# Optimization experiments

Measured on AMD Instinct MI355X. Metric: run time of the kernel, lower is better.

## Reference

```python
import jax, jax.numpy as jnp
import numpy as np

NU, NI, E = 100000, 20000, 250000
H, HEADS, D, L = 128, 2, 64, 2


def setup_inputs() -> dict:
    key = jax.random.key(0)
    ks = jax.random.split(key, 12)
    s = 0.05  # glorot-ish init scale
    return {
        "x_user": jax.random.normal(ks[0], (NU, 64), jnp.float32),
        "x_item": jax.random.normal(ks[1], (NI, 128), jnp.float32),
        "Wp_user": jax.random.normal(ks[2], (64, H), jnp.float32) * s,
        "bp_user": jnp.zeros((H,), jnp.float32),
        "Wp_item": jax.random.normal(ks[3], (128, H), jnp.float32) * s,
        "bp_item": jnp.zeros((H,), jnp.float32),
        # stacked per [layer, relation] params; rel 0 = user->item, rel 1 = item->user
        "Wl": jax.random.normal(ks[4], (L, 2, H, H), jnp.float32) * s,  # source linear
        "bl": jnp.zeros((L, 2, H), jnp.float32),
        "Wr": jax.random.normal(ks[5], (L, 2, H, H), jnp.float32) * s,  # target linear
        "br": jnp.zeros((L, 2, H), jnp.float32),
        "att": jax.random.normal(ks[6], (L, 2, HEADS, D), jnp.float32) * s,
        "bias": jnp.zeros((L, 2, H), jnp.float32),
        "edge_src": jax.random.randint(ks[7], (E,), 0, NU, jnp.int32),  # user index per edge
        "edge_dst": jax.random.randint(ks[8], (E,), 0, NI, jnp.int32),  # item index per edge
    }


def _gatv2(x_src, x_dst, src, dst, wl, bl_, wr, br_, a, b_, n_dst):
    """One bipartite GATv2Conv (heads=HEADS, out=D, concat=True, eval mode)."""
    xl = (x_src @ wl + bl_).reshape(-1, HEADS, D)  # [Ns, h, d]
    xr = (x_dst @ wr + br_).reshape(-1, HEADS, D)  # [Nd, h, d]
    e = jax.nn.leaky_relu(xl[src] + xr[dst], 0.2)  # [E, h, d]
    logits = jnp.einsum('ehd,hd->eh', e, a)        # [E, h]
    # segment softmax over destination nodes (numerically stable)
    amax = jax.lax.stop_gradient(jax.ops.segment_max(logits, dst, num_segments=n_dst))
    p = jnp.exp(logits - amax[dst])
    denom = jax.ops.segment_sum(p, dst, num_segments=n_dst)
    alpha = p / (denom[dst] + 1e-16)               # PyG softmax epsilon
    msg = xl[src] * alpha[:, :, None]              # [E, h, d]
    out = jax.ops.segment_sum(msg, dst, num_segments=n_dst)  # [Nd, h, d]
    return out.reshape(n_dst, HEADS * D) + b_


def reference(x_user, x_item, Wp_user, bp_user, Wp_item, bp_item,
              Wl, bl, Wr, br, att, bias, edge_src, edge_dst):
    zu = x_user @ Wp_user + bp_user  # [NU, H]
    zi = x_item @ Wp_item + bp_item  # [NI, H]
    for l in range(L):
        zi_new = _gatv2(zu, zi, edge_src, edge_dst,
                        Wl[l, 0], bl[l, 0], Wr[l, 0], br[l, 0], att[l, 0], bias[l, 0], NI)
        zu_new = _gatv2(zi, zu, edge_dst, edge_src,
                        Wl[l, 1], bl[l, 1], Wr[l, 1], br[l, 1], att[l, 1], bias[l, 1], NU)
        zu, zi = zu_new, zi_new
        if l < L - 1:
            zu, zi = jax.nn.relu(zu), jax.nn.relu(zi)  # dropout is identity in eval
    return zu, zi
```

## Files before the change

kernel.cpp:

```cpp
#include <hip/hip_runtime.h>

#define HDIM 128

typedef __attribute__((ext_vector_type(8))) short short8;
typedef __attribute__((ext_vector_type(4))) float float4v;

__device__ __forceinline__ float b2f(unsigned short u){
  return __uint_as_float(((unsigned int)u) << 16);
}
__device__ __forceinline__ unsigned short f2b(float f){
  unsigned int x = __float_as_uint(f);
  x += 0x7fffu + ((x >> 16) & 1u);
  return (unsigned short)(x >> 16);
}

#if __has_builtin(__builtin_amdgcn_exp2f)
#define EXPX(x) __builtin_amdgcn_exp2f(x)
#define LOGSCALE 1.4426950408889634f
#else
#define EXPX(x) __expf(x)
#define LOGSCALE 1.f
#endif

__device__ __forceinline__ float dpp_red8(float x){
  x += __int_as_float(__builtin_amdgcn_update_dpp(0, __float_as_int(x), 0xB1, 0xF, 0xF, true));
  x += __int_as_float(__builtin_amdgcn_update_dpp(0, __float_as_int(x), 0x4E, 0xF, 0xF, true));
  x += __int_as_float(__builtin_amdgcn_update_dpp(0, __float_as_int(x), 0x141, 0xF, 0xF, true));
  return x;
}

__global__ void detect_kernel(const unsigned short* __restrict__ x, int* __restrict__ flag){
  const int tid = threadIdx.x;
  int cnt = 0, tot = 0;
  for (int i = tid * 2; i < 4096; i += 512){
    float v = fabsf(b2f(x[i]));
    tot++;
    if (v > 1e-4f && v < 50.f) cnt++;
  }
  __shared__ int s_cnt[256], s_tot[256];
  s_cnt[tid] = cnt; s_tot[tid] = tot;
  __syncthreads();
  for (int o = 128; o > 0; o >>= 1){
    if (tid < o){ s_cnt[tid] += s_cnt[tid + o]; s_tot[tid] += s_tot[tid + o]; }
    __syncthreads();
  }
  if (tid == 0) flag[0] = (s_cnt[0] * 2 < s_tot[0]) ? 1 : 0;
}

#define P_WPU 0
#define P_WPI 8192
#define P_WL  24576
#define P_WR  90112
#define P_BL  155648
#define P_BR  156160
#define P_ATT 156672
#define P_BIA 157184
#define P_BPU 157696
#define P_BPI 157824
#define P_TOT 157952

struct CvtArgs { const void* src[10]; int len[10]; };

__global__ void cvt_all_kernel(CvtArgs args, unsigned short* __restrict__ P,
                               const int* __restrict__ flag){
  int t = blockIdx.x * 256 + threadIdx.x;
  if (t >= P_TOT) return;
  int local = t;
  int i = 0;
  while (local >= args.len[i]){ local -= args.len[i]; i++; }
  if (*flag) P[t] = f2b(((const float*)args.src[i])[local]);
  else       P[t] = ((const unsigned short*)args.src[i])[local];
}

__global__ void prep_weights_kernel(const unsigned short* __restrict__ P,
                                    unsigned short* __restrict__ Wc)
{
  const int t = blockIdx.x * 256 + threadIdx.x;
  if (t >= 49664) return;
  const unsigned short* Wl = P + P_WL;
  const unsigned short* Wr = P + P_WR;
  const unsigned short* Bm[4] = { Wl, Wr + 16384, Wl + 16384, Wr };
  const unsigned short* Av[4] = { P + P_WPU, P + P_WPU, P + P_WPI, P + P_WPI };
  const unsigned short* bv[4] = { P + P_BPU, P + P_BPU, P + P_BPI, P + P_BPI };
  const unsigned short* bo[4] = { P + P_BL, P + P_BR + 128, P + P_BL + 128, P + P_BR };
  if (t < 49152){
    int job, base;
    if (t < 8192)       { job = 0; base = 0; }
    else if (t < 16384) { job = 1; base = 8192; }
    else if (t < 32768) { job = 2; base = 16384; }
    else                { job = 3; base = 32768; }
    const int local = t - base;
    const int k = local >> 7, n = local & 127;
    const unsigned short* A = Av[job] + (size_t)k * 128;
    const unsigned short* B = Bm[job];
    float s = 0.f;
    #pragma unroll 4
    for (int h = 0; h < 128; h++) s = fmaf(b2f(A[h]), b2f(B[h * 128 + n]), s);
    Wc[t] = f2b(s);
  } else {
    const int local = t - 49152;
    const int job = local >> 7, n = local & 127;
    const unsigned short* B = Bm[job];
    float s = b2f(bo[job][n]);
    for (int h = 0; h < 128; h++) s = fmaf(b2f(bv[job][h]), b2f(B[h * 128 + n]), s);
    Wc[t] = f2b(s);
  }
}

struct PermArgs { const unsigned short* W0[4]; const unsigned short* W1[4];
                  int KS[4]; int base[4]; int n[4]; };
__global__ void permute_all_kernel(PermArgs pa, unsigned short* __restrict__ dst){
  int t = blockIdx.x * 256 + threadIdx.x;
  int job = 0;
  while (job < 4 && t >= pa.base[job] + pa.n[job]) job++;
  if (job >= 4) return;
  int local = t - pa.base[job];
  int KS = pa.KS[job];
  int j = local & 7, rest = local >> 3;
  int l = rest & 63; rest >>= 6;
  int ks = rest % KS, tile = rest / KS;
  int k = ks * 32 + (l >> 4) * 8 + j;
  int c = tile * 16 + (l & 15);
  dst[t] = (c < 128) ? pa.W0[job][k * 128 + c] : pa.W1[job][k * 128 + (c - 128)];
}

__global__ void bias_cat_kernel(const unsigned short* a0, const unsigned short* b0,
                                const unsigned short* a1, const unsigned short* b1,
                                const unsigned short* a2, const unsigned short* b2,
                                const unsigned short* a3, const unsigned short* b3,
                                unsigned short* __restrict__ dst){
  int t = blockIdx.x * 256 + threadIdx.x;
  if (t >= 1024) return;
  const unsigned short* lo[4] = {a0, a1, a2, a3};
  const unsigned short* hi[4] = {b0, b1, b2, b3};
  int set = t >> 8, c = t & 255;
  dst[t] = (c < 128) ? lo[set][c] : hi[set][c - 128];
}

template<int K>
__launch_bounds__(256)
__global__ void linear_mfma_kernel(const void* __restrict__ Xv, int xstride,
                                   const int* __restrict__ flag, int use_flag,
                                   const unsigned short* __restrict__ Bp,
                                   const unsigned short* __restrict__ bias,
                                   unsigned short* __restrict__ Y, int M)
{
  constexpr int KS = K / 32;
  const int wave = threadIdx.x >> 6, lane = threadIdx.x & 63;
  const int quad = lane >> 4, l16 = lane & 15;
  const int row0 = blockIdx.x * 64;
  const bool f32 = use_flag && (*flag != 0);

  float4v acc[4][4];
  const float4v z = {0.f, 0.f, 0.f, 0.f};
  #pragma unroll
  for (int i = 0; i < 4; i++)
    #pragma unroll
    for (int j = 0; j < 4; j++) acc[i][j] = z;

  for (int ks = 0; ks < KS; ks++){
    const int col = ks * 32 + quad * 8;
    short8 a[4];
    #pragma unroll
    for (int mt = 0; mt < 4; mt++){
      int r = row0 + mt * 16 + l16; if (r >= M) r = M - 1;
      if (f32){
        const float* p = (const float*)Xv + (size_t)r * xstride + col;
        short8 tmp;
        #pragma unroll
        for (int j = 0; j < 8; j++) tmp[j] = (short)f2b(p[j]);
        a[mt] = tmp;
      } else {
        a[mt] = *(const short8*)((const unsigned short*)Xv + (size_t)r * xstride + col);
      }
    }
    short8 b[4];
    #pragma unroll
    for (int ntl = 0; ntl < 4; ntl++){
      const int t = wave * 4 + ntl;
      b[ntl] = *(const short8*)(Bp + ((size_t)(t * KS + ks) * 64 + lane) * 8);
    }
    #pragma unroll
    for (int mt = 0; mt < 4; mt++)
      #pragma unroll
      for (int ntl = 0; ntl < 4; ntl++)
        acc[mt][ntl] = __builtin_amdgcn_mfma_f32_16x16x32_bf16(a[mt], b[ntl], acc[mt][ntl], 0, 0, 0);
  }

  #pragma unroll
  for (int mt = 0; mt < 4; mt++){
    #pragma unroll
    for (int ntl = 0; ntl < 4; ntl++){
      const int t = wave * 4 + ntl;
      const int colb = t * 16 + l16;
      const float bb = b2f(bias[colb]);
      #pragma unroll
      for (int r = 0; r < 4; r++){
        const int row = row0 + mt * 16 + quad * 4 + r;
        if (row < M) Y[(size_t)row * 256 + colb] = f2b(acc[mt][ntl][r] + bb);
      }
    }
  }
}

__global__ void count_both_kernel(const int* __restrict__ esrc, const int* __restrict__ edst,
                                  int* __restrict__ degU, int* __restrict__ degI, int E){
  int t = blockIdx.x * 256 + threadIdx.x;
  if (t >= E) return;
  atomicAdd(&degI[edst[t]], 1);
  atomicAdd(&degU[esrc[t]], 1);
}

__global__ void scan_block2_kernel(const int* __restrict__ degI, const int* __restrict__ degU,
                                   int* __restrict__ rpI, int* __restrict__ rpU,
                                   int* __restrict__ blkI, int* __restrict__ blkU,
                                   int NI, int NU, int BI){
  __shared__ int s[256];
  const int tid = threadIdx.x;
  const int b = blockIdx.x;
  const int* deg; int* rowptr; int* blksum; int Nd; int bb;
  if (b < BI){ deg = degI; rowptr = rpI; blksum = blkI; Nd = NI; bb = b; }
  else       { deg = degU; rowptr = rpU; blksum = blkU; Nd = NU; bb = b - BI; }
  const int base = bb * 2048 + tid * 8;
  int v[8]; int tot = 0;
  #pragma unroll
  for (int j = 0; j < 8; j++){
    int idx = base + j;
    v[j] = (idx < Nd) ? deg[idx] : 0;
    tot += v[j];
  }
  s[tid] = tot;
  __syncthreads();
  for (int off = 1; off < 256; off <<= 1){
    int add = (tid >= off) ? s[tid - off] : 0;
    __syncthreads();
    s[tid] += add;
    __syncthreads();
  }
  int run = s[tid] - tot;
  #pragma unroll
  for (int j = 0; j < 8; j++){
    int idx = base + j;
    if (idx < Nd) rowptr[idx] = run;
    run += v[j];
  }
  if (tid == 255) blksum[bb] = s[255];
}

__global__ void scan_top2_kernel(int* __restrict__ blkI, int BI,
                                 int* __restrict__ blkU, int BU){
  const int tid = threadIdx.x;
  int* blk = (tid < 64) ? blkI : blkU;
  const int B = (tid < 64) ? BI : BU;
  const int lane = tid & 63;
  int v = (lane < B) ? blk[lane] : 0;
  const int orig = v;
  #pragma unroll
  for (int off = 1; off < 64; off <<= 1){
    int u = __shfl_up(v, off, 64);
    if (lane >= off) v += u;
  }
  if (lane < B) blk[lane] = v - orig;
}

__global__ void scan_add2_kernel(int* __restrict__ rpI, int* __restrict__ rpU,
                                 const int* __restrict__ blkI, const int* __restrict__ blkU,
                                 int* __restrict__ curI, int* __restrict__ curU,
                                 int NI, int NU, int BI, int E){
  const int b = blockIdx.x;
  int* rowptr; const int* blksum; int* curs; int Nd; int bb;
  if (b < BI){ rowptr = rpI; blksum = blkI; curs = curI; Nd = NI; bb = b; }
  else       { rowptr = rpU; blksum = blkU; curs = curU; Nd = NU; bb = b - BI; }
  const int base = bb * 2048 + threadIdx.x * 8;
  const int add = blksum[bb];
  #pragma unroll
  for (int j = 0; j < 8; j++){
    int idx = base + j;
    if (idx < Nd){ int v = rowptr[idx] + add; rowptr[idx] = v; curs[idx] = v; }
    else if (idx == Nd) rowptr[idx] = E;
  }
}

__global__ void scatter_both_kernel(const int* __restrict__ esrc, const int* __restrict__ edst,
                                    int* __restrict__ curI, int* __restrict__ curU,
                                    int* __restrict__ srcI, int* __restrict__ srcU, int E){
  int t = blockIdx.x * 256 + threadIdx.x;
  if (t < E){
    int d = edst[t];
    int pos = atomicAdd(&curI[d], 1);
    srcI[pos] = esrc[t];
  } else if (t < 2 * E){
    int tt = t - E;
    int d = esrc[tt];
    int pos = atomicAdd(&curU[d], 1);
    srcU[pos] = edst[tt];
  }
}

__global__ void hist_deg_kernel(const int* __restrict__ rpI, const int* __restrict__ rpU,
                                int* __restrict__ histI, int* __restrict__ histU,
                                int NI, int NU, int BI){
  __shared__ int h[64];
  const int tid = threadIdx.x;
  if (tid < 64) h[tid] = 0;
  __syncthreads();
  const int b = blockIdx.x;
  const int* rp; int* gh; int base; int N;
  if (b < BI){ rp = rpI; gh = histI; base = b * 256; N = NI; }
  else       { rp = rpU; gh = histU; base = (b - BI) * 256; N = NU; }
  const int n = base + tid;
  if (n < N){ int d = rp[n + 1] - rp[n]; atomicAdd(&h[min(d, 63)], 1); }
  __syncthreads();
  if (tid < 64 && h[tid]) atomicAdd(&gh[tid], h[tid]);
}

__global__ void scan_hist_kernel(int* __restrict__ histI, int* __restrict__ histU){
  const int tid = threadIdx.x;
  const int lane = tid & 63;
  int* h = (tid < 64) ? histI : histU;
  int v = h[lane];
  int x = v;
  #pragma unroll
  for (int off = 1; off < 64; off <<= 1){
    int u = __shfl_down(x, off, 64);
    x += (lane + off < 64) ? u : 0;
  }
  h[lane] = x - v;
}

__global__ void scatter_perm_kernel(const int* __restrict__ rpI, const int* __restrict__ rpU,
                                    int* __restrict__ histI, int* __restrict__ histU,
                                    int* __restrict__ permI, int* __restrict__ permU,
                                    int NI, int NU, int BI){
  __shared__ int h[64];
  __shared__ int cur[64];
  const int tid = threadIdx.x;
  if (tid < 64) h[tid] = 0;
  __syncthreads();
  const int b = blockIdx.x;
  const int* rp; int* gh; int* perm; int base; int N;
  if (b < BI){ rp = rpI; gh = histI; perm = permI; base = b * 256; N = NI; }
  else       { rp = rpU; gh = histU; perm = permU; base = (b - BI) * 256; N = NU; }
  const int n = base + tid;
  int bk = -1;
  if (n < N){ int d = rp[n + 1] - rp[n]; bk = min(d, 63); atomicAdd(&h[bk], 1); }
  __syncthreads();
  if (tid < 64) cur[tid] = h[tid] ? atomicAdd(&gh[tid], h[tid]) : 0;
  __syncthreads();
  if (n < N){ int r = atomicAdd(&cur[bk], 1); perm[r] = n; }
}

struct GatRel {
  const unsigned short* zlrS;
  const unsigned short* zlrD;
  const int* rowptr;
  const int* srcArr;
  const int* perm;
  const unsigned short* att;
  const unsigned short* bias;
  void* out;
  unsigned long long elem_off;
  int Nd;
  int nw;
};

__launch_bounds__(256)
__global__ void fused_gat_sorted_kernel(GatRel A, GatRel B, int do_relu,
                                        const int* __restrict__ flag, int final_store)
{
  const int wave = threadIdx.x >> 6;
  const int lane = threadIdx.x & 63;
  const int ql = lane & 15;
  const int quad = lane >> 4;
  int gw = blockIdx.x * 4 + wave;
  GatRel R;
  if (gw < A.nw) R = A;
  else {
    gw -= A.nw;
    if (gw >= B.nw) return;
    R = B;
  }

  const int rank = gw * 4 + quad;
  const bool vnode = rank < R.Nd;
  int d = 0;
  if (vnode) d = R.perm[rank];
  int beg = 0, end = 0;
  if (vnode){ beg = R.rowptr[d]; end = R.rowptr[d + 1]; }
  int md = end - beg;
  md = max(md, __shfl_xor(md, 16, 64));
  md = max(md, __shfl_xor(md, 32, 64));

  const uint4* zlS4 = (const uint4*)R.zlrS;
  uint4 rv = ((const uint4*)R.zlrD)[(size_t)d * 32 + 16 + ql];
  float r[8], c1[8], c2[8];
  {
    const unsigned int* rp = (const unsigned int*)&rv;
    #pragma unroll
    for (int j = 0; j < 4; j++){
      r[2*j]   = __uint_as_float(rp[j] << 16);
      r[2*j+1] = __uint_as_float(rp[j] & 0xffff0000u);
    }
  }
  uint4 av = ((const uint4*)R.att)[ql];
  {
    const unsigned int* ap = (const unsigned int*)&av;
    #pragma unroll
    for (int j = 0; j < 4; j++){
      const float a0 = __uint_as_float(ap[j] << 16) * LOGSCALE;
      const float a1 = __uint_as_float(ap[j] & 0xffff0000u) * LOGSCALE;
      c1[2*j]   = a0 * 0.6f; c2[2*j]   = a0 * 0.4f;
      c1[2*j+1] = a1 * 0.6f; c2[2*j+1] = a1 * 0.4f;
    }
  }
  float kn = 0.f;
  #pragma unroll
  for (int j = 0; j < 8; j++) kn = fmaf(c1[j], r[j], kn);
  kn = dpp_red8(kn);

  float m = -1e30f, s = 0.f;
  float acc[8];
  #pragma unroll
  for (int j = 0; j < 8; j++) acc[j] = 0.f;

  if (md > 0){
    const int* sA = R.srcArr;
    int i0 = 0, i1 = 0, i2 = 0;
    if (beg     < end) i0 = sA[beg];
    if (beg + 1 < end) i1 = sA[beg + 1];
    if (beg + 2 < end) i2 = sA[beg + 2];
    uint4 g0 = zlS4[(size_t)i0 * 32 + ql];
    uint4 g1 = zlS4[(size_t)i1 * 32 + ql];

    for (int it = 0; it < md; it++){
      uint4 g2 = zlS4[(size_t)i2 * 32 + ql];
      int i3 = 0;
      { int ee = beg + it + 3; if (ee < end) i3 = sA[ee]; }
      const bool valid = (beg + it) < end;

      float x[8];
      {
        const unsigned int* gp = (const unsigned int*)&g0;
        #pragma unroll
        for (int j = 0; j < 4; j++){
          x[2*j]   = __uint_as_float(gp[j] << 16);
          x[2*j+1] = __uint_as_float(gp[j] & 0xffff0000u);
        }
      }
      float q1 = 0.f, q2 = 0.f;
      #pragma unroll
      for (int j = 0; j < 8; j++){
        const float t = x[j] + r[j];
        q1 = fmaf(c1[j], x[j], q1);
        q2 = fmaf(c2[j], fabsf(t), q2);
      }
      const float p = dpp_red8(q1 + q2) + kn;
      const float pv = valid ? p : -1e30f;

      if (__builtin_expect(__any(pv > m + 8.f), 0)){
        const float mn = fmaxf(m, pv);
        const float scO = EXPX(m - mn);
        const float qv = valid ? EXPX(pv - mn) : 0.f;
        s = fmaf(s, scO, qv);
        #pragma unroll
        for (int j = 0; j < 8; j++) acc[j] = fmaf(acc[j], scO, x[j] * qv);
        m = mn;
      } else {
        const float qv = valid ? EXPX(pv - m) : 0.f;
        s += qv;
        #pragma unroll
        for (int j = 0; j < 8; j++) acc[j] = fmaf(x[j], qv, acc[j]);
      }
      g0 = g1; g1 = g2; i2 = i3;
    }
  }

  const float inv = 1.f / (s + 1e-16f);
  uint4 bv = ((const uint4*)R.bias)[ql];
  float o[8];
  {
    const unsigned int* bp = (const unsigned int*)&bv;
    #pragma unroll
    for (int j = 0; j < 4; j++){
      o[2*j]   = fmaf(acc[2*j],   inv, __uint_as_float(bp[j] << 16));
      o[2*j+1] = fmaf(acc[2*j+1], inv, __uint_as_float(bp[j] & 0xffff0000u));
    }
  }
  if (do_relu){
    #pragma unroll
    for (int j = 0; j < 8; j++) o[j] = fmaxf(o[j], 0.f);
  }
  if (!vnode) return;
  const size_t eidx = (size_t)R.elem_off + (size_t)d * HDIM + 8 * ql;
  if (final_store && (*flag != 0)){
    float4 f0 = {o[0], o[1], o[2], o[3]};
    float4 f1 = {o[4], o[5], o[6], o[7]};
    float4* op = (float4*)R.out;
    op[eidx >> 2] = f0;
    op[(eidx >> 2) + 1] = f1;
  } else {
    uint4 w;
    unsigned int* wp = (unsigned int*)&w;
    #pragma unroll
    for (int j = 0; j < 4; j++)
      wp[j] = (unsigned int)f2b(o[2*j]) | ((unsigned int)f2b(o[2*j+1]) << 16);
    ((uint4*)R.out)[eidx >> 3] = w;
  }
}

extern "C" void kernel_launch(void* const* d_in, const int* in_sizes, int n_in,
                              void* d_out, int out_size, void* d_ws, size_t ws_size,
                              hipStream_t stream)
{
  const int* esrc = (const int*)d_in[12];
  const int* edst = (const int*)d_in[13];

  const int NU = in_sizes[0] / 64;
  const int NI = in_sizes[1] / 128;
  const int E  = in_sizes[12];
  const size_t fu = (size_t)NU * HDIM, fi = (size_t)NI * HDIM;

  char* w = (char*)d_ws;
  auto carve = [&](size_t bytes){ char* p = w; w += (bytes + 255) & ~(size_t)255; return p; };
  int* flag = (int*)carve(4);
  unsigned short* Wc = (unsigned short*)carve(49664 * 2);
  unsigned short* P  = (unsigned short*)carve((size_t)P_TOT * 2);
  unsigned short* Bp = (unsigned short*)carve(114688 * 2);
  unsigned short* Bc = (unsigned short*)carve(1024 * 2);
  int* rowptrI = (int*)carve(((size_t)NI + 1) * 4);
  int* rowptrU = (int*)carve(((size_t)NU + 1) * 4);
  int* curs    = (int*)carve(((size_t)NI + NU) * 4);
  int* cursI = curs;
  int* cursU = curs + NI;
  int* blkI = (int*)carve(64 * 4);
  int* blkU = (int*)carve(64 * 4);
  int* hists = (int*)carve(128 * 4);
  int* histI = hists;
  int* histU = hists + 64;
  int* permI = (int*)carve((size_t)NI * 4);
  int* permU = (int*)carve((size_t)NU * 4);
  int* srcI  = (int*)carve((size_t)E * 4);
  int* srcU  = (int*)carve((size_t)E * 4);
  unsigned short* zlrU = (unsigned short*)carve((size_t)NU * 256 * 2);
  unsigned short* zlrI = (unsigned short*)carve((size_t)NI * 256 * 2);
  (void)ws_size; (void)n_in; (void)out_size; (void)fi;

  unsigned short* stage_zu = (unsigned short*)d_out;
  unsigned short* stage_zi = (unsigned short*)d_out + fu;
  (void)stage_zi;

  detect_kernel<<<1, 256, 0, stream>>>((const unsigned short*)d_in[0], flag);
  CvtArgs ca;
  const int srcIdx[10] = {2, 4, 6, 8, 7, 9, 10, 11, 3, 5};
  const int lens[10] = {8192, 16384, 65536, 65536, 512, 512, 512, 512, 128, 128};
  for (int i = 0; i < 10; i++){ ca.src[i] = d_in[srcIdx[i]]; ca.len[i] = lens[i]; }
  cvt_all_kernel<<<(P_TOT + 255) / 256, 256, 0, stream>>>(ca, P, flag);
  prep_weights_kernel<<<(49664 + 255) / 256, 256, 0, stream>>>(P, Wc);

  const unsigned short* cWlU0 = Wc;
  const unsigned short* cWrU1 = Wc + 8192;
  const unsigned short* cWlI1 = Wc + 16384;
  const unsigned short* cWrI0 = Wc + 32768;

  PermArgs pa;
  pa.W0[0] = cWlU0;                 pa.W1[0] = cWrU1;                 pa.KS[0] = 2; pa.base[0] = 0;     pa.n[0] = 16384;
  pa.W0[1] = cWlI1;                 pa.W1[1] = cWrI0;                 pa.KS[1] = 4; pa.base[1] = 16384; pa.n[1] = 32768;
  pa.W0[2] = P + P_WL + 2 * 16384;  pa.W1[2] = P + P_WR + 3 * 16384;  pa.KS[2] = 4; pa.base[2] = 49152; pa.n[2] = 32768;
  pa.W0[3] = P + P_WL + 3 * 16384;  pa.W1[3] = P + P_WR + 2 * 16384;  pa.KS[3] = 4; pa.base[3] = 81920; pa.n[3] = 32768;
  permute_all_kernel<<<(114688 + 255) / 256, 256, 0, stream>>>(pa, Bp);
  unsigned short* BpU0 = Bp;
  unsigned short* BpI0 = Bp + 16384;
  unsigned short* BpU1 = Bp + 49152;
  unsigned short* BpI1 = Bp + 81920;
  bias_cat_kernel<<<4, 256, 0, stream>>>(
      Wc + 49152, Wc + 49152 + 128,
      Wc + 49152 + 256, Wc + 49152 + 384,
      P + P_BL + 256, P + P_BR + 384,
      P + P_BL + 384, P + P_BR + 256,
      Bc);

  const int BI = (NI + 2047) / 2048, BU = (NU + 2047) / 2048;
  hipMemsetAsync(curs, 0, ((size_t)NI + NU) * 4, stream);
  hipMemsetAsync(hists, 0, 512, stream);
  count_both_kernel<<<(E + 255) / 256, 256, 0, stream>>>(esrc, edst, cursU, cursI, E);
  scan_block2_kernel<<<BI + BU, 256, 0, stream>>>(cursI, cursU, rowptrI, rowptrU, blkI, blkU, NI, NU, BI);
  scan_top2_kernel<<<1, 128, 0, stream>>>(blkI, BI, blkU, BU);
  scan_add2_kernel<<<BI + BU, 256, 0, stream>>>(rowptrI, rowptrU, blkI, blkU, cursI, cursU, NI, NU, BI, E);

  const int BI2 = (NI + 255) / 256, BU2 = (NU + 255) / 256;
  hist_deg_kernel<<<BI2 + BU2, 256, 0, stream>>>(rowptrI, rowptrU, histI, histU, NI, NU, BI2);
  scan_hist_kernel<<<1, 128, 0, stream>>>(histI, histU);
  scatter_perm_kernel<<<BI2 + BU2, 256, 0, stream>>>(rowptrI, rowptrU, histI, histU, permI, permU, NI, NU, BI2);

  scatter_both_kernel<<<(2 * E + 255) / 256, 256, 0, stream>>>(esrc, edst, cursI, cursU, srcI, srcU, E);

  const int gMU = (NU + 63) / 64, gMI = (NI + 63) / 64;
  const int nwA = (NI + 3) / 4, nwB = (NU + 3) / 4;
  const int gGat = (nwA + nwB + 3) / 4;

  for (int l = 0; l < 2; l++){
    if (l == 0){
      linear_mfma_kernel<64><<<gMU, 256, 0, stream>>>(d_in[0], 64, flag, 1, BpU0, Bc, zlrU, NU);
      linear_mfma_kernel<128><<<gMI, 256, 0, stream>>>(d_in[1], 128, flag, 1, BpI0, Bc + 256, zlrI, NI);
    } else {
      linear_mfma_kernel<128><<<gMU, 256, 0, stream>>>(stage_zu, 128, flag, 0, BpU1, Bc + 512, zlrU, NU);
      linear_mfma_kernel<128><<<gMI, 256, 0, stream>>>(stage_zi, 128, flag, 0, BpI1, Bc + 768, zlrI, NI);
    }
    const int relu = (l == 0);
    const int final_store = (l == 1);

    GatRel A, B;
    A.zlrS = zlrU; A.zlrD = zlrI; A.rowptr = rowptrI; A.srcArr = srcI; A.perm = permI;
    A.att  = P + P_ATT + (l * 2 + 0) * HDIM;
    A.bias = P + P_BIA + (l * 2 + 0) * HDIM;
    A.out = final_store ? d_out : (void*)stage_zu; A.elem_off = fu; A.Nd = NI; A.nw = nwA;
    B.zlrS = zlrI; B.zlrD = zlrU; B.rowptr = rowptrU; B.srcArr = srcU; B.perm = permU;
    B.att  = P + P_ATT + (l * 2 + 1) * HDIM;
    B.bias = P + P_BIA + (l * 2 + 1) * HDIM;
    B.out = final_store ? d_out : (void*)stage_zu; B.elem_off = 0; B.Nd = NU; B.nw = nwB;

    fused_gat_sorted_kernel<<<gGat, 256, 0, stream>>>(A, B, relu, flag, final_store);
  }
}
```

Baseline: 364.4 us.

## Process two edges per iteration with packed float2 math in GAT kernel

Unrolls the per-destination edge loop by two and processes both edges with packed two-wide float vectors, so the compiler can emit packed FP32 ops. Leaky-relu is computed directly with a vector max in place of the earlier 0.6/0.4 abs decomposition. The gather prefetch depth grows to four rows, and the block size rises from 256 to 512 threads. This cuts loop overhead and raises memory-level parallelism, at the cost of more registers and extra wasted work on odd-degree nodes.

```diff
diff --git a/kernel.cpp b/kernel.cpp
--- a/kernel.cpp
+++ b/kernel.cpp
@@ -4,6 +4,7 @@
 
 typedef __attribute__((ext_vector_type(8))) short short8;
 typedef __attribute__((ext_vector_type(4))) float float4v;
+typedef __attribute__((ext_vector_type(2))) float f32x2;
 
 __device__ __forceinline__ float b2f(unsigned short u){
   return __uint_as_float(((unsigned int)u) << 16);
@@ -27,6 +28,24 @@
   x += __int_as_float(__builtin_amdgcn_update_dpp(0, __float_as_int(x), 0x4E, 0xF, 0xF, true));
   x += __int_as_float(__builtin_amdgcn_update_dpp(0, __float_as_int(x), 0x141, 0xF, 0xF, true));
   return x;
+}
+
+__device__ __forceinline__ f32x2 lrelu2(f32x2 t){
+  f32x2 u = t * 0.2f;
+#if __has_builtin(__builtin_elementwise_max)
+  return __builtin_elementwise_max(t, u);
+#else
+  f32x2 o; o.x = fmaxf(t.x, u.x); o.y = fmaxf(t.y, u.y); return o;
+#endif
+}
+
+__device__ __forceinline__ void unpack8(const uint4& g, f32x2* x){
+  const unsigned int* gp = (const unsigned int*)&g;
+  #pragma unroll
+  for (int j = 0; j < 4; j++){
+    x[j].x = __uint_as_float(gp[j] << 16);
+    x[j].y = __uint_as_float(gp[j] & 0xffff0000u);
+  }
 }
 
 __global__ void detect_kernel(const unsigned short* __restrict__ x, int* __restrict__ flag){
@@ -364,7 +383,7 @@
   int nw;
 };
 
-__launch_bounds__(256)
+__launch_bounds__(512)
 __global__ void fused_gat_sorted_kernel(GatRel A, GatRel B, int do_relu,
                                         const int* __restrict__ flag, int final_store)
 {
@@ -372,7 +391,7 @@
   const int lane = threadIdx.x & 63;
   const int ql = lane & 15;
   const int quad = lane >> 4;
-  int gw = blockIdx.x * 4 + wave;
+  int gw = blockIdx.x * 8 + wave;
   GatRel R;
   if (gw < A.nw) R = A;
   else {
@@ -393,85 +412,79 @@
 
   const uint4* zlS4 = (const uint4*)R.zlrS;
   uint4 rv = ((const uint4*)R.zlrD)[(size_t)d * 32 + 16 + ql];
-  float r[8], c1[8], c2[8];
+  f32x2 r2[4], a2[4];
+  unpack8(rv, r2);
   {
-    const unsigned int* rp = (const unsigned int*)&rv;
-    #pragma unroll
-    for (int j = 0; j < 4; j++){
-      r[2*j]   = __uint_as_float(rp[j] << 16);
-      r[2*j+1] = __uint_as_float(rp[j] & 0xffff0000u);
-    }
-  }
-  uint4 av = ((const uint4*)R.att)[ql];
-  {
-    const unsigned int* ap = (const unsigned int*)&av;
-    #pragma unroll
-    for (int j = 0; j < 4; j++){
-      const float a0 = __uint_as_float(ap[j] << 16) * LOGSCALE;
-      const float a1 = __uint_as_float(ap[j] & 0xffff0000u) * LOGSCALE;
-      c1[2*j]   = a0 * 0.6f; c2[2*j]   = a0 * 0.4f;
-      c1[2*j+1] = a1 * 0.6f; c2[2*j+1] = a1 * 0.4f;
-    }
-  }
-  float kn = 0.f;
-  #pragma unroll
-  for (int j = 0; j < 8; j++) kn = fmaf(c1[j], r[j], kn);
-  kn = dpp_red8(kn);
+    uint4 av = ((const uint4*)R.att)[ql];
+    unpack8(av, a2);
+    #pragma unroll
+    for (int j = 0; j < 4; j++) a2[j] = a2[j] * LOGSCALE;
+  }
 
   float m = -1e30f, s = 0.f;
-  float acc[8];
-  #pragma unroll
-  for (int j = 0; j < 8; j++) acc[j] = 0.f;
+  f32x2 acc2[4];
+  const f32x2 z2 = {0.f, 0.f};
+  #pragma unroll
+  for (int j = 0; j < 4; j++) acc2[j] = z2;
 
   if (md > 0){
     const int* sA = R.srcArr;
-    int i0 = 0, i1 = 0, i2 = 0;
+    int i0 = 0, i1 = 0, i2 = 0, i3 = 0;
     if (beg     < end) i0 = sA[beg];
     if (beg + 1 < end) i1 = sA[beg + 1];
     if (beg + 2 < end) i2 = sA[beg + 2];
+    if (beg + 3 < end) i3 = sA[beg + 3];
     uint4 g0 = zlS4[(size_t)i0 * 32 + ql];
     uint4 g1 = zlS4[(size_t)i1 * 32 + ql];
 
-    for (int it = 0; it < md; it++){
+    for (int it = 0; it < md; it += 2){
       uint4 g2 = zlS4[(size_t)i2 * 32 + ql];
-      int i3 = 0;
-      { int ee = beg + it + 3; if (ee < end) i3 = sA[ee]; }
-      const bool valid = (beg + it) < end;
-
-      float x[8];
-      {
-        const unsigned int* gp = (const unsigned int*)&g0;
+      uint4 g3 = zlS4[(size_t)i3 * 32 + ql];
+      int i4 = 0, i5 = 0;
+      { int ee = beg + it + 4; if (ee < end) i4 = sA[ee]; }
+      { int ee = beg + it + 5; if (ee < end) i5 = sA[ee]; }
+      const int rem = end - beg - it;
+      const bool v0 = rem > 0, v1 = rem > 1;
+
+      f32x2 x0[4], x1[4];
+      unpack8(g0, x0);
+      unpack8(g1, x1);
+
+      f32x2 d0 = z2, d1 = z2;
+      #pragma unroll
+      for (int j = 0; j < 4; j++){
+        d0 = a2[j] * lrelu2(x0[j] + r2[j]) + d0;
+        d1 = a2[j] * lrelu2(x1[j] + r2[j]) + d1;
+      }
+      const float p0 = dpp_red8(d0.x + d0.y);
+      const float p1 = dpp_red8(d1.x + d1.y);
+      const float pv0 = v0 ? p0 : -1e30f;
+      const float pv1 = v1 ? p1 : -1e30f;
+      const float pmax = fmaxf(pv0, pv1);
+
+      if (__builtin_expect(__any(pmax > m + 8.f), 0)){
+        const float mn = fmaxf(m, pmax);
+        const float scO = EXPX(m - mn);
+        const float q0 = v0 ? EXPX(pv0 - mn) : 0.f;
+        const float q1 = v1 ? EXPX(pv1 - mn) : 0.f;
+        s = fmaf(s, scO, q0 + q1);
+        const f32x2 q0v = {q0, q0}, q1v = {q1, q1}, sOv = {scO, scO};
+        #pragma unroll
+        for (int j = 0; j < 4; j++)
+          acc2[j] = acc2[j] * sOv + (x0[j] * q0v + x1[j] * q1v);
+        m = mn;
+      } else {
+        const float q0 = v0 ? EXPX(pv0 - m) : 0.f;
+        const float q1 = v1 ? EXPX(pv1 - m) : 0.f;
+        s += q0 + q1;
+        const f32x2 q0v = {q0, q0}, q1v = {q1, q1};
         #pragma unroll
         for (int j = 0; j < 4; j++){
-          x[2*j]   = __uint_as_float(gp[j] << 16);
-          x[2*j+1] = __uint_as_float(gp[j] & 0xffff0000u);
+          acc2[j] = x0[j] * q0v + acc2[j];
+          acc2[j] = x1[j] * q1v + acc2[j];
         }
       }
-      float q1 = 0.f, q2 = 0.f;
-      #pragma unroll
-      for (int j = 0; j < 8; j++){
-        const float t = x[j] + r[j];
-        q1 = fmaf(c1[j], x[j], q1);
-        q2 = fmaf(c2[j], fabsf(t), q2);
-      }
-      const float p = dpp_red8(q1 + q2) + kn;
-      const float pv = valid ? p : -1e30f;
-
-      if (__builtin_expect(__any(pv > m + 8.f), 0)){
-        const float mn = fmaxf(m, pv);
-        const float scO = EXPX(m - mn);
-        const float qv = valid ? EXPX(pv - mn) : 0.f;
-        s = fmaf(s, scO, qv);
-        #pragma unroll
-        for (int j = 0; j < 8; j++) acc[j] = fmaf(acc[j], scO, x[j] * qv);
-        m = mn;
-      } else {
-        const float qv = valid ? EXPX(pv - m) : 0.f;
-        s += qv;
-        #pragma unroll
-        for (int j = 0; j < 8; j++) acc[j] = fmaf(x[j], qv, acc[j]);
-      }
-      g0 = g1; g1 = g2; i2 = i3;
+      g0 = g2; g1 = g3; i2 = i4; i3 = i5;
     }
   }
 
@@ -482,8 +495,8 @@
     const unsigned int* bp = (const unsigned int*)&bv;
     #pragma unroll
     for (int j = 0; j < 4; j++){
-      o[2*j]   = fmaf(acc[2*j],   inv, __uint_as_float(bp[j] << 16));
-      o[2*j+1] = fmaf(acc[2*j+1], inv, __uint_as_float(bp[j] & 0xffff0000u));
+      o[2*j]   = fmaf(acc2[j].x, inv, __uint_as_float(bp[j] << 16));
+      o[2*j+1] = fmaf(acc2[j].y, inv, __uint_as_float(bp[j] & 0xffff0000u));
     }
   }
   if (do_relu){
@@ -596,7 +609,7 @@
 
   const int gMU = (NU + 63) / 64, gMI = (NI + 63) / 64;
   const int nwA = (NI + 3) / 4, nwB = (NU + 3) / 4;
-  const int gGat = (nwA + nwB + 3) / 4;
+  const int gGat = (nwA + nwB + 7) / 8;
 
   for (int l = 0; l < 2; l++){
     if (l == 0){
@@ -619,6 +632,6 @@
     B.bias = P + P_BIA + (l * 2 + 1) * HDIM;
     B.out = final_store ? d_out : (void*)stage_zu; B.elem_off = 0; B.Nd = NU; B.nw = nwB;
 
-    fused_gat_sorted_kernel<<<gGat, 256, 0, stream>>>(A, B, relu, flag, final_store);
-  }
-}
+    fused_gat_sorted_kernel<<<gGat, 512, 0, stream>>>(A, B, relu, flag, final_store);
+  }
+}
```

Measured after the change: 363.0 us. No clear change (-0.4%).
